# Optimization experiments

Hardware: AMD Instinct MI355X
Metric: run time of the kernel (lower is better)

Reference implementation:

```python
import jax, jax.numpy as jnp
import numpy as np
from jax import lax

WIN = 5
EPS = 1e-08
SHAPE = (2, 1, 160, 192, 224)


def _box1d(x, axis, win):
    """Sliding-window sum of size `win` along `axis`, zero-padded (same size).
    Uses a cumsum difference -> O(1) work per voxel instead of dense conv."""
    pad = win // 2
    pw = [(0, 0)] * x.ndim
    pw[axis] = (pad + 1, pad)
    c = jnp.cumsum(jnp.pad(x, pw), axis=axis)
    n = x.shape[axis]
    hi = lax.slice_in_dim(c, win, win + n, axis=axis)
    lo = lax.slice_in_dim(c, 0, n, axis=axis)
    return hi - lo


def _box_sum3d(x, win):
    for axis in (2, 3, 4):
        x = _box1d(x, axis, win)
    return x


def setup_inputs() -> dict:
    key = jax.random.key(0)
    k1, k2, k3 = jax.random.split(key, 3)
    I = jax.random.uniform(k1, SHAPE, dtype=jnp.float32)
    J = jax.random.uniform(k2, SHAPE, dtype=jnp.float32)
    weight_map = jax.random.uniform(k3, SHAPE, dtype=jnp.float32)
    return {"I": I, "J": J, "weight_map": weight_map}


def reference(I, J, weight_map):
    win = WIN
    win_size = float(win ** 3)
    I_sum = _box_sum3d(I, win)
    J_sum = _box_sum3d(J, win)
    I2_sum = _box_sum3d(I * I, win)
    J2_sum = _box_sum3d(J * J, win)
    IJ_sum = _box_sum3d(I * J, win)
    u_I = I_sum / win_size
    u_J = J_sum / win_size
    cross = IJ_sum - u_J * I_sum - u_I * J_sum + u_I * u_J * win_size
    I_var = I2_sum - 2.0 * u_I * I_sum + u_I * u_I * win_size
    J_var = J2_sum - 2.0 * u_J * J_sum + u_J * u_J * win_size
    cc = cross * cross / (I_var * J_var + EPS)
    return -1.0 * jnp.mean(cc * weight_map)
```

## Files before the change

kernel.cpp:

```cpp
#include <hip/hip_runtime.h>

#define N_  2
#define D_  160
#define H_  192
#define W_  224
#define TW  32
#define TH  16
#define ZCH 32
#define NZC (D_/ZCH)
#define HR  (TH+4)
#define HC  (TW+4)
#define PL  (H_*W_)
#define TOT (N_*D_*H_*W_)

#define BAR() asm volatile("s_waitcnt lgkmcnt(0)\n\ts_barrier" ::: "memory")

__global__ __launch_bounds__(256, 4) void ncc_kernel(
    const float* __restrict__ I, const float* __restrict__ J,
    const float* __restrict__ Wm, float* __restrict__ out)
{
    __shared__ __align__(16) float zsL[5][HR][HC];
    __shared__ __align__(16) float sx [5][HR][HC];
    __shared__ float red[4];

    const int tid = threadIdx.x;
    const int bx = blockIdx.x, by = blockIdx.y;
    const int n  = blockIdx.z / NZC;
    const int c0 = (blockIdx.z % NZC) * ZCH;
    const int nbase = n * D_ * PL;

    const bool aAct = tid < 180;
    const int arow = tid / 9;
    const int ag   = tid % 9;
    const int ah   = by * TH - 2 + arow;
    const int ahc  = min(max(ah, 0), H_ - 1);
    const int aw0  = bx * TW - 2 + 4 * ag;
    const bool mH  = (ah == ahc);
    const bool mW0 = (aw0 >= 0);
    const bool mW1 = (aw0 + 3 < W_);
    const int awc0 = max(aw0, 0);
    const int awc1 = min(aw0 + 2, W_ - 4);
    const int preA0 = nbase + ahc * W_ + awc0;
    const int preA1 = nbase + ahc * W_ + awc1;

    const bool bAct = tid < 160;
    const int brow = tid >> 3;
    const int bxo  = (tid & 7) * 4;

    const int cty = tid >> 4;
    const int cx0 = (tid & 15) * 2;
    const int ch  = by * TH + cty;
    const int cw  = bx * TW + cx0;
    const int preW = nbase + ch * W_ + cw;

    float rI[4][5], rJ[4][5], zs[5][4];
#pragma unroll
    for (int c = 0; c < 4; ++c)
#pragma unroll
        for (int k = 0; k < 5; ++k) { rI[c][k] = 0.f; rJ[c][k] = 0.f; }
#pragma unroll
    for (int a = 0; a < 5; ++a)
#pragma unroll
        for (int c = 0; c < 4; ++c) zs[a][c] = 0.f;

    float acc = 0.f;
    const float inv125 = 1.0f / 125.0f;

    float cI[4] = {0.f,0.f,0.f,0.f}, cJ[4] = {0.f,0.f,0.f,0.f};
    {
        const int z0 = c0 - 2;
        const int zc = min(max(z0, 0), D_ - 1);
        const bool mZ = (z0 == zc);
        const int zoff = zc * PL;
        if (aAct) {
            const float2 i0 = *(const float2*)&I[preA0 + zoff];
            const float2 i1 = *(const float2*)&I[preA1 + zoff];
            const float2 j0 = *(const float2*)&J[preA0 + zoff];
            const float2 j1 = *(const float2*)&J[preA1 + zoff];
            const float f0 = (mH && mW0 && mZ) ? 1.f : 0.f;
            const float f1 = (mH && mW1 && mZ) ? 1.f : 0.f;
            cI[0]=i0.x*f0; cI[1]=i0.y*f0; cI[2]=i1.x*f1; cI[3]=i1.y*f1;
            cJ[0]=j0.x*f0; cJ[1]=j0.y*f0; cJ[2]=j1.x*f1; cJ[3]=j1.y*f1;
        }
    }
    float wmCx = 0.f, wmCy = 0.f;

    for (int s = 0; s < ZCH + 4; ++s) {
        const int zn  = c0 - 1 + s;
        const int znc = min(max(zn, 0), D_ - 1);
        const bool mZn = (zn == znc);
        const int zoffn = znc * PL;
        float2 pi0, pi1, pj0, pj1;
        if (aAct) {
            pi0 = *(const float2*)&I[preA0 + zoffn];
            pi1 = *(const float2*)&I[preA1 + zoffn];
            pj0 = *(const float2*)&J[preA0 + zoffn];
            pj1 = *(const float2*)&J[preA1 + zoffn];
        } else {
            pi0 = pi1 = pj0 = pj1 = make_float2(0.f, 0.f);
        }
        const int zon  = c0 - 3 + s;
        const int zonc = min(max(zon, 0), D_ - 1);
        const float2 wmN = *(const float2*)&Wm[preW + zonc * PL];

        if (aAct) {
#pragma unroll
            for (int c = 0; c < 4; ++c) {
                const float vi = cI[c], vj = cJ[c];
                const float oi = rI[c][0], oj = rJ[c][0];
                zs[0][c] += vi - oi;
                zs[1][c] += vj - oj;
                zs[2][c] += vi*vi - oi*oi;
                zs[3][c] += vj*vj - oj*oj;
                zs[4][c] += vi*vj - oi*oj;
#pragma unroll
                for (int k = 0; k < 4; ++k) { rI[c][k]=rI[c][k+1]; rJ[c][k]=rJ[c][k+1]; }
                rI[c][4] = vi; rJ[c][4] = vj;
            }
#pragma unroll
            for (int a = 0; a < 5; ++a)
                *(float4*)&zsL[a][arow][4*ag] =
                    make_float4(zs[a][0], zs[a][1], zs[a][2], zs[a][3]);
        }
        BAR();

        if (bAct) {
#pragma unroll
            for (int a = 0; a < 5; ++a) {
                const float4 v0 = *(const float4*)&zsL[a][brow][bxo];
                const float4 v1 = *(const float4*)&zsL[a][brow][bxo + 4];
                const float m  = v0.y + v0.z + v0.w;
                const float u1 = v1.x + v1.y;
                const float u2 = u1 + v1.z;
                *(float4*)&sx[a][brow][bxo] =
                    make_float4(v0.x + m + v1.x, m + u1,
                                (v0.z + v0.w) + u2, v0.w + (u2 + v1.w));
            }
        }
        BAR();

        if (s >= 4) {
            float2 S[5];
#pragma unroll
            for (int a = 0; a < 5; ++a) {
                float2 v = *(const float2*)&sx[a][cty][cx0];
#pragma unroll
                for (int k = 1; k < 5; ++k) {
                    const float2 w = *(const float2*)&sx[a][cty + k][cx0];
                    v.x += w.x; v.y += w.y;
                }
                S[a] = v;
            }
            {
                const float cr = S[4].x - S[0].x * S[1].x * inv125;
                const float vi = S[2].x - S[0].x * S[0].x * inv125;
                const float vj = S[3].x - S[1].x * S[1].x * inv125;
                acc += wmCx * (cr * cr) * __builtin_amdgcn_rcpf(vi * vj + 1e-8f);
            }
            {
                const float cr = S[4].y - S[0].y * S[1].y * inv125;
                const float vi = S[2].y - S[0].y * S[0].y * inv125;
                const float vj = S[3].y - S[1].y * S[1].y * inv125;
                acc += wmCy * (cr * cr) * __builtin_amdgcn_rcpf(vi * vj + 1e-8f);
            }
        }

        {
            const float f0 = (mH && mW0 && mZn) ? 1.f : 0.f;
            const float f1 = (mH && mW1 && mZn) ? 1.f : 0.f;
            cI[0]=pi0.x*f0; cI[1]=pi0.y*f0; cI[2]=pi1.x*f1; cI[3]=pi1.y*f1;
            cJ[0]=pj0.x*f0; cJ[1]=pj0.y*f0; cJ[2]=pj1.x*f1; cJ[3]=pj1.y*f1;
        }
        wmCx = wmN.x; wmCy = wmN.y;
    }

#pragma unroll
    for (int off = 32; off > 0; off >>= 1)
        acc += __shfl_down(acc, off, 64);
    const int wave = tid >> 6;
    const int lane = tid & 63;
    if (lane == 0) red[wave] = acc;
    __syncthreads();
    if (tid == 0) {
        const float t = red[0] + red[1] + red[2] + red[3];
        atomicAdd(out, t * (-1.0f / (float)TOT));
    }
}

extern "C" void kernel_launch(void* const* d_in, const int* in_sizes, int n_in,
                              void* d_out, int out_size, void* d_ws, size_t ws_size,
                              hipStream_t stream)
{
    const float* I  = (const float*)d_in[0];
    const float* J  = (const float*)d_in[1];
    const float* Wm = (const float*)d_in[2];
    float* out = (float*)d_out;

    hipMemsetAsync(out, 0, sizeof(float), stream);

    dim3 grid(W_ / TW, H_ / TH, N_ * NZC);
    dim3 block(256);
    hipLaunchKernelGGL(ncc_kernel, grid, block, 0, stream, I, J, Wm, out);
}
```

Before: 201.6 us.

## Halve z-chunk and compute two output rows per thread with sliding H-sum

The z-chunk per block shrinks from 32 to 16 slices, which doubles the grid size but raises the share of halo work (4 extra slices per chunk). In the final stage, 128 threads each compute two adjacent output rows. The second row's 5-row sum is built from the first by subtracting one row and adding the next, which cuts LDS reads. The goal is more parallelism and fewer shared-memory loads in the last stage, traded against extra redundant z-halo loads and compute, and half the threads idling in that stage.

```diff
diff --git a/kernel.cpp b/kernel.cpp
--- a/kernel.cpp
+++ b/kernel.cpp
@@ -6,7 +6,7 @@
 #define W_  224
 #define TW  32
 #define TH  16
-#define ZCH 32
+#define ZCH 16
 #define NZC (D_/ZCH)
 #define HR  (TH+4)
 #define HC  (TW+4)
@@ -47,11 +47,13 @@
     const int brow = tid >> 3;
     const int bxo  = (tid & 7) * 4;
 
-    const int cty = tid >> 4;
+    const bool cAct = tid < 128;
+    const int crp = tid >> 4;
+    const int cr0 = 2 * crp;
     const int cx0 = (tid & 15) * 2;
-    const int ch  = by * TH + cty;
+    const int ch0 = by * TH + cr0;
     const int cw  = bx * TW + cx0;
-    const int preW = nbase + ch * W_ + cw;
+    const int preW = nbase + ch0 * W_ + cw;
 
     float rI[4][5], rJ[4][5], zs[5][4];
 #pragma unroll
@@ -83,7 +85,7 @@
             cJ[0]=j0.x*f0; cJ[1]=j0.y*f0; cJ[2]=j1.x*f1; cJ[3]=j1.y*f1;
         }
     }
-    float wmCx = 0.f, wmCy = 0.f;
+    float wm0x=0.f, wm0y=0.f, wm1x=0.f, wm1y=0.f;
 
     for (int s = 0; s < ZCH + 4; ++s) {
         const int zn  = c0 - 1 + s;
@@ -99,9 +101,13 @@
         } else {
             pi0 = pi1 = pj0 = pj1 = make_float2(0.f, 0.f);
         }
-        const int zon  = c0 - 3 + s;
-        const int zonc = min(max(zon, 0), D_ - 1);
-        const float2 wmN = *(const float2*)&Wm[preW + zonc * PL];
+        float2 wmN0 = make_float2(0.f, 0.f), wmN1 = make_float2(0.f, 0.f);
+        if (cAct) {
+            const int zon  = c0 - 3 + s;
+            const int zonc = min(max(zon, 0), D_ - 1);
+            wmN0 = *(const float2*)&Wm[preW + zonc * PL];
+            wmN1 = *(const float2*)&Wm[preW + W_ + zonc * PL];
+        }
 
         if (aAct) {
 #pragma unroll
@@ -139,29 +145,42 @@
         }
         BAR();
 
-        if (s >= 4) {
-            float2 S[5];
+        if (cAct && s >= 4) {
+            float2 ST[5], SB[5];
 #pragma unroll
             for (int a = 0; a < 5; ++a) {
-                float2 v = *(const float2*)&sx[a][cty][cx0];
-#pragma unroll
-                for (int k = 1; k < 5; ++k) {
-                    const float2 w = *(const float2*)&sx[a][cty + k][cx0];
-                    v.x += w.x; v.y += w.y;
-                }
-                S[a] = v;
+                const float2 r0 = *(const float2*)&sx[a][cr0    ][cx0];
+                const float2 r1 = *(const float2*)&sx[a][cr0 + 1][cx0];
+                const float2 r2 = *(const float2*)&sx[a][cr0 + 2][cx0];
+                const float2 r3 = *(const float2*)&sx[a][cr0 + 3][cx0];
+                const float2 r4 = *(const float2*)&sx[a][cr0 + 4][cx0];
+                const float2 r5 = *(const float2*)&sx[a][cr0 + 5][cx0];
+                float2 t;
+                t.x = ((r0.x + r1.x) + (r2.x + r3.x)) + r4.x;
+                t.y = ((r0.y + r1.y) + (r2.y + r3.y)) + r4.y;
+                ST[a] = t;
+                SB[a] = make_float2(t.x - r0.x + r5.x,
+                                    t.y - r0.y + r5.y);
             }
             {
-                const float cr = S[4].x - S[0].x * S[1].x * inv125;
-                const float vi = S[2].x - S[0].x * S[0].x * inv125;
-                const float vj = S[3].x - S[1].x * S[1].x * inv125;
-                acc += wmCx * (cr * cr) * __builtin_amdgcn_rcpf(vi * vj + 1e-8f);
+                const float crx = ST[4].x - ST[0].x * ST[1].x * inv125;
+                const float vix = ST[2].x - ST[0].x * ST[0].x * inv125;
+                const float vjx = ST[3].x - ST[1].x * ST[1].x * inv125;
+                acc += wm0x * (crx * crx) * __builtin_amdgcn_rcpf(vix * vjx + 1e-8f);
+                const float cry = ST[4].y - ST[0].y * ST[1].y * inv125;
+                const float viy = ST[2].y - ST[0].y * ST[0].y * inv125;
+                const float vjy = ST[3].y - ST[1].y * ST[1].y * inv125;
+                acc += wm0y * (cry * cry) * __builtin_amdgcn_rcpf(viy * vjy + 1e-8f);
             }
             {
-                const float cr = S[4].y - S[0].y * S[1].y * inv125;
-                const float vi = S[2].y - S[0].y * S[0].y * inv125;
-                const float vj = S[3].y - S[1].y * S[1].y * inv125;
-                acc += wmCy * (cr * cr) * __builtin_amdgcn_rcpf(vi * vj + 1e-8f);
+                const float crx = SB[4].x - SB[0].x * SB[1].x * inv125;
+                const float vix = SB[2].x - SB[0].x * SB[0].x * inv125;
+                const float vjx = SB[3].x - SB[1].x * SB[1].x * inv125;
+                acc += wm1x * (crx * crx) * __builtin_amdgcn_rcpf(vix * vjx + 1e-8f);
+                const float cry = SB[4].y - SB[0].y * SB[1].y * inv125;
+                const float viy = SB[2].y - SB[0].y * SB[0].y * inv125;
+                const float vjy = SB[3].y - SB[1].y * SB[1].y * inv125;
+                acc += wm1y * (cry * cry) * __builtin_amdgcn_rcpf(viy * vjy + 1e-8f);
             }
         }
 
@@ -171,7 +190,7 @@
             cI[0]=pi0.x*f0; cI[1]=pi0.y*f0; cI[2]=pi1.x*f1; cI[3]=pi1.y*f1;
             cJ[0]=pj0.x*f0; cJ[1]=pj0.y*f0; cJ[2]=pj1.x*f1; cJ[3]=pj1.y*f1;
         }
-        wmCx = wmN.x; wmCy = wmN.y;
+        wm0x = wmN0.x; wm0y = wmN0.y; wm1x = wmN1.x; wm1y = wmN1.y;
     }
 
 #pragma unroll
```

Measured after the change: 257.9 us. 27.9% more time.
